# Performance work log

Hardware: AMD Instinct MI355X
Metric: run time of the kernel (lower is better)

Reference implementation:

```python
import jax, jax.numpy as jnp
import numpy as np

N_NODES = 50000
N_EDGES = 800000
D_IN = 128
D_H = 128
N_LAYERS = 3
N_CLASSES = 10
NUM_GRAPHS = 256
BN_EPS = 1e-5


def _bn(h, gamma, beta):
    # BatchNorm1d, training-mode statistics (biased variance) over node axis
    mu = jnp.mean(h, axis=0)
    var = jnp.mean((h - mu) ** 2, axis=0)
    return (h - mu) * jax.lax.rsqrt(var + BN_EPS) * gamma + beta


def setup_inputs() -> dict:
    key = jax.random.key(0)
    ks = jax.random.split(key, 16)
    x = jax.random.normal(ks[0], (N_NODES, D_IN), dtype=jnp.float32)
    edge_index = jax.random.randint(ks[1], (2, N_EDGES), 0, N_NODES, dtype=jnp.int64)
    batch = jnp.sort(jax.random.randint(ks[2], (N_NODES,), 0, NUM_GRAPHS, dtype=jnp.int64))
    s1 = 1.0 / np.sqrt(D_IN)
    s2 = 1.0 / np.sqrt(D_H)
    W1 = jax.random.uniform(ks[3], (N_LAYERS, D_IN, D_H), jnp.float32, -s1, s1)
    b1 = jax.random.uniform(ks[4], (N_LAYERS, D_H), jnp.float32, -s1, s1)
    g1 = jnp.ones((N_LAYERS, D_H), jnp.float32)
    bt1 = jnp.zeros((N_LAYERS, D_H), jnp.float32)
    W2 = jax.random.uniform(ks[5], (N_LAYERS, D_H, D_H), jnp.float32, -s2, s2)
    b2 = jax.random.uniform(ks[6], (N_LAYERS, D_H), jnp.float32, -s2, s2)
    g2 = jnp.ones((N_LAYERS, D_H), jnp.float32)
    bt2 = jnp.zeros((N_LAYERS, D_H), jnp.float32)
    sc = 1.0 / np.sqrt(D_H * N_LAYERS)
    Wc1 = jax.random.uniform(ks[7], (D_H * N_LAYERS, D_H), jnp.float32, -sc, sc)
    bc1 = jax.random.uniform(ks[8], (D_H,), jnp.float32, -sc, sc)
    Wc2 = jax.random.uniform(ks[9], (D_H, N_CLASSES), jnp.float32, -s2, s2)
    bc2 = jax.random.uniform(ks[10], (N_CLASSES,), jnp.float32, -s2, s2)
    return {"x": x, "edge_index": edge_index, "batch": batch,
            "W1": W1, "b1": b1, "g1": g1, "bt1": bt1,
            "W2": W2, "b2": b2, "g2": g2, "bt2": bt2,
            "Wc1": Wc1, "bc1": bc1, "Wc2": Wc2, "bc2": bc2}


def reference(x, edge_index, batch, W1, b1, g1, bt1, W2, b2, g2, bt2, Wc1, bc1, Wc2, bc2):
    src = edge_index[0]
    dst = edge_index[1]
    readouts = []
    h = x
    for i in range(N_LAYERS):
        # GINConv, eps=0: (1+eps)*h + sum_{j->i} h_j, then MLP
        agg = jax.ops.segment_sum(h[src], dst, num_segments=N_NODES)  # [N, d]
        z = h + agg
        z = z @ W1[i] + b1[i]
        z = jax.nn.relu(_bn(z, g1[i], bt1[i]))
        z = z @ W2[i] + b2[i]
        # outer BN + ReLU
        h = jax.nn.relu(_bn(z, g2[i], bt2[i]))
        readouts.append(jax.ops.segment_sum(h, batch, num_segments=NUM_GRAPHS))
    h_graph = jnp.concatenate(readouts, axis=1)  # [G, L*d]
    # classifier (dropout in eval mode -> identity)
    out = jax.nn.relu(h_graph @ Wc1 + bc1) @ Wc2 + bc2
    return out
```

## Files before the change

### kernel.cpp

```cpp
#include <hip/hip_runtime.h>

#define N_NODES 50000
#define N_EDGES 800000
#define D 128
#define NLAYERS 3
#define N_CLASSES 10
#define NUM_GRAPHS 256
#define BN_EPS 1e-5f

#define CHUNKS 64
#define CHSIZE 12500
#define RANGES 4
#define RSIZE 12500
#define SBANKS 8
#define NBLK 196

typedef __attribute__((ext_vector_type(4))) float f4;
typedef __attribute__((ext_vector_type(2))) float f2;
typedef __attribute__((ext_vector_type(4))) int i4;
typedef __attribute__((ext_vector_type(8))) short short8;
typedef __attribute__((ext_vector_type(4))) unsigned short us4;
typedef __attribute__((ext_vector_type(8))) unsigned short us8;

__device__ inline float b2f(unsigned short u) {
    unsigned int i = ((unsigned int)u) << 16;
    return __builtin_bit_cast(float, i);
}
__device__ inline unsigned short f2b(float f) {
    unsigned int u = __builtin_bit_cast(unsigned int, f);
    unsigned int r = (u + 0x7FFFu + ((u >> 16) & 1u)) >> 16;
    return (unsigned short)r;
}

__device__ inline void coef_to_lds(const float* __restrict__ stats,
                                   const float* __restrict__ g,
                                   const float* __restrict__ bt,
                                   float* ac_sm, int tid) {
    if (tid < D) {
        float s = 0.f, q = 0.f;
#pragma unroll
        for (int b = 0; b < SBANKS; b++) {
            s += stats[b * 2 * D + tid];
            q += stats[b * 2 * D + D + tid];
        }
        float mu = s * (1.0f / N_NODES);
        float var = q * (1.0f / N_NODES) - mu * mu;
        float inv = rsqrtf(var + BN_EPS);
        float a = g[tid] * inv;
        ac_sm[tid] = a;
        ac_sm[D + tid] = bt[tid] - mu * a;
    }
}


__global__ __launch_bounds__(256) void k_ph(const int* __restrict__ dst,
                                            unsigned short* __restrict__ pos,
                                            unsigned short* __restrict__ ph) {
    __shared__ int h[RSIZE];
    int c = blockIdx.x, r = blockIdx.y;
    int t = threadIdx.x;
    for (int i = t; i < RSIZE; i += 256) h[i] = 0;
    __syncthreads();
    int base = c * CHSIZE;
    int lo = r * RSIZE;
    const i4* dst4 = (const i4*)(dst + base);
    for (int j = t; j < CHSIZE / 4; j += 256) {
        i4 dv = dst4[j];
#pragma unroll
        for (int u = 0; u < 4; u++) {
            int d = dv[u] - lo;
            if ((unsigned)d < RSIZE) pos[base + j * 4 + u] = (unsigned short)atomicAdd(&h[d], 1);
        }
    }
    __syncthreads();
    unsigned short* outp = ph + (size_t)c * N_NODES + lo;
    for (int i = t; i < RSIZE; i += 256) outp[i] = (unsigned short)h[i];
}

__global__ __launch_bounds__(256) void k_m1(unsigned short* __restrict__ ph,
                                            const int* __restrict__ bat,
                                            int* __restrict__ deg,
                                            int* __restrict__ bsum,
                                            int* __restrict__ gp,
                                            int* __restrict__ bh) {
    __shared__ int sm[256];
    __shared__ int hist[64];
    int t = threadIdx.x;
    if (t < 64) hist[t] = 0;
    int b = blockIdx.x * 256 + t;
    int s = 0;
    if (b < N_NODES) {
#pragma unroll 4
        for (int c = 0; c < CHUNKS; c++) {
            int v = ph[(size_t)c * N_NODES + b];
            ph[(size_t)c * N_NODES + b] = (unsigned short)s;
            s += v;
        }
        deg[b] = s;
    }
    sm[t] = s;
    __syncthreads();
    if (b < N_NODES) atomicAdd(&hist[min(s, 63)], 1);
    for (int off = 128; off > 0; off >>= 1) {
        if (t < off) sm[t] += sm[t + off];
        __syncthreads();
    }
    if (t == 0) bsum[blockIdx.x] = sm[0];
    if (t < 64) bh[blockIdx.x * 64 + t] = hist[t];
    if (b < N_NODES) {
        int bb = bat[b];
        int prev = (b == 0) ? -1 : bat[b - 1];
        for (int g = prev + 1; g <= bb; g++) gp[g] = b;
        if (b == N_NODES - 1)
            for (int g = bb + 1; g <= NUM_GRAPHS; g++) gp[g] = N_NODES;
    }
}


__global__ __launch_bounds__(256) void k_xw(const float* __restrict__ x,
                                            const float* __restrict__ W1,
                                            const float* __restrict__ W2,
                                            us4* __restrict__ xb,
                                            short8* __restrict__ Wb) {
    int gid = blockIdx.x * 256 + threadIdx.x;
    const f4* xf = (const f4*)x;
#pragma unroll
    for (int rep = 0; rep < 2; rep++) {
        int i = gid + rep * 800000;
        f4 v = xf[i];
        us4 o;
        o[0] = f2b(v.x); o[1] = f2b(v.y); o[2] = f2b(v.z); o[3] = f2b(v.w);
        xb[i] = o;
    }
    if (gid < 6 * 32 * 64) {
        int m = gid >> 11;
        int f = (gid >> 6) & 31;
        int l = gid & 63;
        int ct = f >> 2, ks = f & 3;
        int n = ct * 16 + (l & 15);
        int k0 = ks * 32 + (l >> 4) * 8;
        const float* Wsrc = (m < 3) ? (W1 + (size_t)m * D * D) : (W2 + (size_t)(m - 3) * D * D);
        short8 o;
#pragma unroll
        for (int j = 0; j < 8; j++) o[j] = (short)f2b(Wsrc[(size_t)(k0 + j) * D + n]);
        Wb[gid] = o;
    }
}


__global__ void k_s2(int* __restrict__ bsum, int* __restrict__ rowp, int* __restrict__ bh) {
    __shared__ int sm[256];
    int t = threadIdx.x;
    int v = (t < NBLK) ? bsum[t] : 0;
    sm[t] = v;
    __syncthreads();
    for (int off = 1; off < 256; off <<= 1) {
        int u = (t >= off) ? sm[t - off] : 0;
        __syncthreads();
        sm[t] += u;
        __syncthreads();
    }
    if (t < NBLK) bsum[t] = sm[t] - v;
    if (t == NBLK - 1) rowp[N_NODES] = sm[t];
    __syncthreads();
    int tot = 0;
    if (t < 64) {
        for (int blk = 0; blk < NBLK; blk++) tot += bh[blk * 64 + t];
    }
    sm[t] = (t < 64) ? tot : 0;
    __syncthreads();
    for (int off = 1; off < 64; off <<= 1) {
        int u = (t >= off && t < 64) ? sm[t - off] : 0;
        __syncthreads();
        if (t < 64) sm[t] += u;
        __syncthreads();
    }
    if (t < 64) {
        int run = sm[t] - tot;
        for (int blk = 0; blk < NBLK; blk++) {
            int tmp = bh[blk * 64 + t];
            bh[blk * 64 + t] = run;
            run += tmp;
        }
    }
}


__global__ void k_s3(const int* __restrict__ deg, const int* __restrict__ bsum,
                     int* __restrict__ rowp, const int* __restrict__ bh,
                     unsigned short* __restrict__ perm) {
    __shared__ int sm[256];
    __shared__ int lh[64];
    int t = threadIdx.x;
    if (t < 64) lh[t] = 0;
    int i = blockIdx.x * 256 + t;
    int v = (i < N_NODES) ? deg[i] : 0;
    sm[t] = v;
    __syncthreads();
    for (int off = 1; off < 256; off <<= 1) {
        int u = (t >= off) ? sm[t - off] : 0;
        __syncthreads();
        sm[t] += u;
        __syncthreads();
    }
    if (i < N_NODES) {
        rowp[i] = bsum[blockIdx.x] + sm[t] - v;
        int bk = min(v, 63);
        int p = atomicAdd(&lh[bk], 1);
        perm[bh[blockIdx.x * 64 + bk] + p] = (unsigned short)i;
    }
}

__global__ __launch_bounds__(256) void k_scatter(const int* __restrict__ src,
                                                 const int* __restrict__ dst,
                                                 const unsigned short* __restrict__ pos,
                                                 const unsigned short* __restrict__ ph,
                                                 const int* __restrict__ rowp,
                                                 unsigned short* __restrict__ csr) {
    int e0 = (blockIdx.x * 256 + threadIdx.x) * 4;
    if (e0 >= N_EDGES) return;
    i4 sv = *(const i4*)(src + e0);
    i4 dv = *(const i4*)(dst + e0);
    us4 pv = *(const us4*)(pos + e0);
#pragma unroll
    for (int u = 0; u < 4; u++) {
        int cc = (e0 + u) / CHSIZE;
        int d = dv[u];
        csr[rowp[d] + (int)ph[(size_t)cc * N_NODES + d] + (int)pv[u]] = (unsigned short)sv[u];
    }
}


template <bool APPLY_T>
__global__ __launch_bounds__(256) void k_agg(const us8* __restrict__ H,
                                             const float* __restrict__ stats,
                                             const float* __restrict__ g,
                                             const float* __restrict__ bt,
                                             const int* __restrict__ rowp,
                                             const unsigned short* __restrict__ csr,
                                             const unsigned short* __restrict__ perm,
                                             us8* __restrict__ U) {
    __shared__ float ac_sm[2 * D];
    int tid = threadIdx.x;
    if (APPLY_T) {
        coef_to_lds(stats, g, bt, ac_sm, tid);
        __syncthreads();
    }
    int gid = blockIdx.x * 256 + tid;
    int node = perm[gid >> 4];
    int lane = tid & 15;
    float av[8], cv[8];
    if (APPLY_T) {
#pragma unroll
        for (int i = 0; i < 8; i++) {
            av[i] = ac_sm[lane * 8 + i];
            cv[i] = ac_sm[D + lane * 8 + i];
        }
    }
    float s[8] = {0.f, 0.f, 0.f, 0.f, 0.f, 0.f, 0.f, 0.f};
    auto accum = [&](us8 v) {
#pragma unroll
        for (int i = 0; i < 8; i++) {
            float f = b2f(v[i]);
            if (APPLY_T) f = fmaxf(f * av[i] + cv[i], 0.f);
            s[i] += f;
        }
    };
    accum(H[(size_t)node * 16 + lane]);
    int beg = rowp[node], end = rowp[node + 1];
    int j = beg;
    for (; j + 8 <= end; j += 8) {
        int idx[8];
#pragma unroll
        for (int u = 0; u < 8; u++) idx[u] = csr[j + u];
        us8 v[8];
#pragma unroll
        for (int u = 0; u < 8; u++) v[u] = H[(size_t)idx[u] * 16 + lane];
#pragma unroll
        for (int u = 0; u < 8; u++) accum(v[u]);
    }
    for (; j + 2 <= end; j += 2) {
        int i0 = csr[j], i1 = csr[j + 1];
        us8 v0 = H[(size_t)i0 * 16 + lane];
        us8 v1 = H[(size_t)i1 * 16 + lane];
        accum(v0); accum(v1);
    }
    if (j < end) accum(H[(size_t)csr[j] * 16 + lane]);
    us8 o;
#pragma unroll
    for (int i = 0; i < 8; i++) o[i] = f2b(s[i]);
    U[(size_t)node * 16 + lane] = o;
}


template <bool TRANS>
__global__ __launch_bounds__(256) void k_gemm(const unsigned short* __restrict__ A,
                                              const short8* __restrict__ Wb,
                                              const float* __restrict__ bias,
                                              const float* __restrict__ stats_in,
                                              const float* __restrict__ g,
                                              const float* __restrict__ bt,
                                              unsigned short* __restrict__ Z,
                                              float* __restrict__ stats_out, int M) {
    __shared__ float lds_s[D], lds_q[D];
    __shared__ float ac_sm[2 * D];
    int tid = threadIdx.x;
    if (tid < D) { lds_s[tid] = 0.f; lds_q[tid] = 0.f; }
    if (TRANS) coef_to_lds(stats_in, g, bt, ac_sm, tid);
    int w = tid >> 6, l = tid & 63;
    int lr = l & 15, lg = l >> 4;
    int rowb0 = blockIdx.x * 128 + w * 32;
    f4 acc[2][8];
#pragma unroll
    for (int ct = 0; ct < 8; ct++) {
        float bv = bias[ct * 16 + lr];
#pragma unroll
        for (int rt = 0; rt < 2; rt++) {
            acc[rt][ct].x = bv; acc[rt][ct].y = bv; acc[rt][ct].z = bv; acc[rt][ct].w = bv;
        }
    }
    __syncthreads();

#pragma unroll
    for (int ks = 0; ks < 4; ks++) {
        short8 a[2];
#pragma unroll
        for (int rt = 0; rt < 2; rt++) {
            int arow = rowb0 + rt * 16 + lr;
            int arow_c = arow < M ? arow : M - 1;
            if (!TRANS) {
                a[rt] = *(const short8*)(A + (size_t)arow_c * D + ks * 32 + lg * 8);
            } else {
                int k0 = ks * 32 + lg * 8;
                const unsigned short* ap = A + (size_t)arow_c * D + k0;
                us4 v0 = *(const us4*)ap;
                us4 v1 = *(const us4*)(ap + 4);
                f4 a0 = *(const f4*)&ac_sm[k0];
                f4 a1 = *(const f4*)&ac_sm[k0 + 4];
                f4 c0 = *(const f4*)&ac_sm[D + k0];
                f4 c1 = *(const f4*)&ac_sm[D + k0 + 4];
                a[rt][0] = (short)f2b(fmaxf(b2f(v0[0]) * a0.x + c0.x, 0.f));
                a[rt][1] = (short)f2b(fmaxf(b2f(v0[1]) * a0.y + c0.y, 0.f));
                a[rt][2] = (short)f2b(fmaxf(b2f(v0[2]) * a0.z + c0.z, 0.f));
                a[rt][3] = (short)f2b(fmaxf(b2f(v0[3]) * a0.w + c0.w, 0.f));
                a[rt][4] = (short)f2b(fmaxf(b2f(v1[0]) * a1.x + c1.x, 0.f));
                a[rt][5] = (short)f2b(fmaxf(b2f(v1[1]) * a1.y + c1.y, 0.f));
                a[rt][6] = (short)f2b(fmaxf(b2f(v1[2]) * a1.z + c1.z, 0.f));
                a[rt][7] = (short)f2b(fmaxf(b2f(v1[3]) * a1.w + c1.w, 0.f));
            }
        }
#pragma unroll
        for (int ct = 0; ct < 8; ct++) {
            short8 b = Wb[(ct * 4 + ks) * 64 + l];
            acc[0][ct] = __builtin_amdgcn_mfma_f32_16x16x32_bf16(a[0], b, acc[0][ct], 0, 0, 0);
            acc[1][ct] = __builtin_amdgcn_mfma_f32_16x16x32_bf16(a[1], b, acc[1][ct], 0, 0, 0);
        }
    }

#pragma unroll
    for (int ct = 0; ct < 8; ct++) {
        float s = 0.f, q = 0.f;
#pragma unroll
        for (int rt = 0; rt < 2; rt++) {
#pragma unroll
            for (int r = 0; r < 4; r++) {
                float v = acc[rt][ct][r];
                int rd = rowb0 + rt * 16 + lg * 4 + r;
                float m = rd < M ? 1.f : 0.f;
                s += v * m;
                q += v * v * m;
                if (rd < M) Z[(size_t)rd * D + ct * 16 + lr] = f2b(v);
            }
        }
        s += __shfl_xor(s, 16);
        s += __shfl_xor(s, 32);
        q += __shfl_xor(q, 16);
        q += __shfl_xor(q, 32);
        if (lg == 0) {
            atomicAdd(&lds_s[ct * 16 + lr], s);
            atomicAdd(&lds_q[ct * 16 + lr], q);
        }
    }
    __syncthreads();
    int bank = blockIdx.x & (SBANKS - 1);
    if (tid < D) {
        atomicAdd(&stats_out[bank * 2 * D + tid], lds_s[tid]);
        atomicAdd(&stats_out[bank * 2 * D + D + tid], lds_q[tid]);
    }
}


__global__ __launch_bounds__(256) void k_readout(const unsigned int* __restrict__ Zb,
                                                 const float* __restrict__ stats,
                                                 const float* __restrict__ g,
                                                 const float* __restrict__ bt,
                                                 const int* __restrict__ gp,
                                                 const int* __restrict__ batch,
                                                 float* __restrict__ ro, int layer) {
    __shared__ f2 sm[256];
    __shared__ float ac_sm[2 * D];
    int tid = threadIdx.x;
    coef_to_lds(stats, g, bt, ac_sm, tid);
    __syncthreads();
    int n0 = blockIdx.x * 256;
    int n1 = n0 + 256; if (n1 > N_NODES) n1 = N_NODES;
    int g_lo = batch[n0], g_hi = batch[n1 - 1];
    int grp = tid >> 6, cw = tid & 63;
    float a0 = ac_sm[2 * cw], a1 = ac_sm[2 * cw + 1];
    float c0 = ac_sm[D + 2 * cw], c1 = ac_sm[D + 2 * cw + 1];
    for (int gg = g_lo; gg <= g_hi; gg++) {
        int beg = gp[gg]; if (beg < n0) beg = n0;
        int end = gp[gg + 1]; if (end > n1) end = n1;
        f2 acc; acc.x = 0.f; acc.y = 0.f;
        for (int r = beg + grp; r < end; r += 4) {
            unsigned int v = Zb[(size_t)r * 64 + cw];
            float x0 = b2f((unsigned short)(v & 0xFFFFu));
            float x1 = b2f((unsigned short)(v >> 16));
            acc.x += fmaxf(x0 * a0 + c0, 0.f);
            acc.y += fmaxf(x1 * a1 + c1, 0.f);
        }
        sm[tid] = acc;
        __syncthreads();
        if (tid < 64) {
            f2 t = sm[tid];
            t.x += sm[tid + 64].x + sm[tid + 128].x + sm[tid + 192].x;
            t.y += sm[tid + 64].y + sm[tid + 128].y + sm[tid + 192].y;
            atomicAdd(&ro[(size_t)gg * (NLAYERS * D) + layer * D + 2 * cw], t.x);
            atomicAdd(&ro[(size_t)gg * (NLAYERS * D) + layer * D + 2 * cw + 1], t.y);
        }
        __syncthreads();
    }
}


__global__ void k_cls(const float* __restrict__ ro, const float* __restrict__ Wc1,
                      const float* __restrict__ bc1, const float* __restrict__ Wc2,
                      const float* __restrict__ bc2, float* __restrict__ out) {
    __shared__ float r_sm[NLAYERS * D];
    __shared__ float h_sm[D];
    int g = blockIdx.x;
    int t = threadIdx.x;
    for (int i = t; i < NLAYERS * D; i += D) r_sm[i] = ro[(size_t)g * (NLAYERS * D) + i];
    __syncthreads();
    float acc = bc1[t];
    for (int k = 0; k < NLAYERS * D; k++) acc += r_sm[k] * Wc1[(size_t)k * D + t];
    h_sm[t] = fmaxf(acc, 0.f);
    __syncthreads();
    if (t < N_CLASSES) {
        float o = bc2[t];
        for (int k = 0; k < D; k++) o += h_sm[k] * Wc2[k * N_CLASSES + t];
        out[g * N_CLASSES + t] = o;
    }
}


extern "C" void kernel_launch(void* const* d_in, const int* in_sizes, int n_in,
                              void* d_out, int out_size, void* d_ws, size_t ws_size,
                              hipStream_t stream) {
    const float* x   = (const float*)d_in[0];
    const int*   ei  = (const int*)d_in[1];
    const int*   bat = (const int*)d_in[2];
    const float* W1  = (const float*)d_in[3];
    const float* b1  = (const float*)d_in[4];
    const float* g1  = (const float*)d_in[5];
    const float* bt1 = (const float*)d_in[6];
    const float* W2  = (const float*)d_in[7];
    const float* b2  = (const float*)d_in[8];
    const float* g2  = (const float*)d_in[9];
    const float* bt2 = (const float*)d_in[10];
    const float* Wc1 = (const float*)d_in[11];
    const float* bc1 = (const float*)d_in[12];
    const float* Wc2 = (const float*)d_in[13];
    const float* bc2 = (const float*)d_in[14];
    float* out = (float*)d_out;

    const int* src = ei;
    const int* dst = ei + N_EDGES;

    char* ws = (char*)d_ws;
    size_t off = 0;
    auto alloc = [&](size_t bytes) -> void* {
        void* p = ws + off;
        off += (bytes + 255) & ~(size_t)255;
        return p;
    };
    float* stats = (float*)alloc(6 * SBANKS * 2 * D * sizeof(float));
    float* ro    = (float*)alloc((size_t)NUM_GRAPHS * NLAYERS * D * sizeof(float));
    size_t zero_bytes = off;
    int*   deg   = (int*)alloc(N_NODES * sizeof(int));
    int*   gp    = (int*)alloc((NUM_GRAPHS + 1) * sizeof(int));
    int*   bsum  = (int*)alloc(256 * sizeof(int));
    int*   rowp  = (int*)alloc((N_NODES + 1) * sizeof(int));
    int*   bh    = (int*)alloc(NBLK * 64 * sizeof(int));
    unsigned short* pos  = (unsigned short*)alloc(N_EDGES * sizeof(unsigned short));
    unsigned short* csr  = (unsigned short*)alloc(N_EDGES * sizeof(unsigned short));
    unsigned short* perm = (unsigned short*)alloc(N_NODES * sizeof(unsigned short));
    const size_t NBH = (size_t)N_NODES * D * sizeof(unsigned short);
    unsigned short* xb   = (unsigned short*)alloc(NBH);
    unsigned short* bufA = (unsigned short*)alloc(NBH);
    unsigned short* bufB = (unsigned short*)alloc(NBH);
    unsigned short* bufC = (unsigned short*)alloc(NBH);
    short8* Wb   = (short8*)alloc(6 * 32 * 64 * sizeof(short8));
    unsigned short* ph = (unsigned short*)bufB;

    hipMemsetAsync(ws, 0, zero_bytes, stream);

    k_ph<<<dim3(CHUNKS, RANGES), 256, 0, stream>>>(dst, pos, ph);
    k_m1<<<NBLK, 256, 0, stream>>>(ph, bat, deg, bsum, gp, bh);
    k_xw<<<3125, 256, 0, stream>>>(x, W1, W2, (us4*)xb, Wb);
    k_s2<<<1, 256, 0, stream>>>(bsum, rowp, bh);
    k_s3<<<NBLK, 256, 0, stream>>>(deg, bsum, rowp, bh, perm);
    k_scatter<<<(N_EDGES / 4 + 255) / 256, 256, 0, stream>>>(src, dst, pos, ph, rowp, csr);

    const int agg_grid  = N_NODES * 16 / 256;
    const int gemm_grid = (N_NODES + 127) / 128;
    const unsigned short* H = xb;
    for (int i = 0; i < NLAYERS; i++) {
        float* st1 = stats + (size_t)(2 * i) * SBANKS * 2 * D;
        float* st2 = stats + (size_t)(2 * i + 1) * SBANKS * 2 * D;
        float* st2p = stats + (size_t)(2 * i - 1) * SBANKS * 2 * D;
        if (i == 0)
            k_agg<false><<<agg_grid, 256, 0, stream>>>((const us8*)H, nullptr, nullptr, nullptr,
                                                       rowp, csr, perm, (us8*)bufA);
        else
            k_agg<true><<<agg_grid, 256, 0, stream>>>((const us8*)H, st2p, g2 + (i - 1) * D,
                                                      bt2 + (i - 1) * D, rowp, csr, perm, (us8*)bufA);
        k_gemm<false><<<gemm_grid, 256, 0, stream>>>(bufA, Wb + (size_t)i * 2048, b1 + i * D,
                                                     nullptr, nullptr, nullptr, bufB, st1, N_NODES);
        k_gemm<true><<<gemm_grid, 256, 0, stream>>>(bufB, Wb + (size_t)(3 + i) * 2048, b2 + i * D,
                                                    st1, g1 + i * D, bt1 + i * D, bufC, st2, N_NODES);
        k_readout<<<NBLK, 256, 0, stream>>>((const unsigned int*)bufC, st2, g2 + i * D, bt2 + i * D,
                                            gp, bat, ro, i);
        H = bufC;
    }
    k_cls<<<NUM_GRAPHS, 128, 0, stream>>>(ro, Wc1, bc1, Wc2, bc2, out);
}
```

Measured before the change: 334.2 us.

## Fuse neighbor aggregation with first MLP GEMM via LDS tile

Merges the aggregation kernel and the first GEMM of each layer into one kernel. Each block aggregates 128 nodes in perm order into an LDS tile, then runs MFMA on that tile, scatters rows to their original node positions, and accumulates batch-norm statistics. This removes one launch per layer and the round trip of the aggregated buffer through global memory. In exchange, the output writes become scattered, 128 nodes are aggregated per block with less parallelism, and LDS use grows. The scatter kernel also hoists the chunk index computation out of its loop.

```diff
diff --git a/kernel.cpp b/kernel.cpp
--- a/kernel.cpp
+++ b/kernel.cpp
@@ -14,6 +14,7 @@
 #define RSIZE 12500
 #define SBANKS 8
 #define NBLK 196
+#define UP 136
 
 typedef __attribute__((ext_vector_type(4))) float f4;
 typedef __attribute__((ext_vector_type(2))) float f2;
@@ -219,36 +220,41 @@
                                                  unsigned short* __restrict__ csr) {
     int e0 = (blockIdx.x * 256 + threadIdx.x) * 4;
     if (e0 >= N_EDGES) return;
+    int cc = e0 / CHSIZE;
     i4 sv = *(const i4*)(src + e0);
     i4 dv = *(const i4*)(dst + e0);
     us4 pv = *(const us4*)(pos + e0);
+    const unsigned short* phc = ph + (size_t)cc * N_NODES;
 #pragma unroll
     for (int u = 0; u < 4; u++) {
-        int cc = (e0 + u) / CHSIZE;
         int d = dv[u];
-        csr[rowp[d] + (int)ph[(size_t)cc * N_NODES + d] + (int)pv[u]] = (unsigned short)sv[u];
+        csr[rowp[d] + (int)phc[d] + (int)pv[u]] = (unsigned short)sv[u];
     }
 }
 
 
 template <bool APPLY_T>
-__global__ __launch_bounds__(256) void k_agg(const us8* __restrict__ H,
-                                             const float* __restrict__ stats,
-                                             const float* __restrict__ g,
-                                             const float* __restrict__ bt,
-                                             const int* __restrict__ rowp,
-                                             const unsigned short* __restrict__ csr,
-                                             const unsigned short* __restrict__ perm,
-                                             us8* __restrict__ U) {
+__global__ __launch_bounds__(256) void k_ag(const us8* __restrict__ H,
+                                            const float* __restrict__ stats,
+                                            const float* __restrict__ g,
+                                            const float* __restrict__ bt,
+                                            const int* __restrict__ rowp,
+                                            const unsigned short* __restrict__ csr,
+                                            const unsigned short* __restrict__ perm,
+                                            const short8* __restrict__ Wb,
+                                            const float* __restrict__ bias,
+                                            unsigned short* __restrict__ Z,
+                                            float* __restrict__ stats_out) {
+    __shared__ unsigned short u[128][UP];
     __shared__ float ac_sm[2 * D];
+    __shared__ float lds_s[D], lds_q[D];
     int tid = threadIdx.x;
-    if (APPLY_T) {
-        coef_to_lds(stats, g, bt, ac_sm, tid);
-        __syncthreads();
-    }
-    int gid = blockIdx.x * 256 + tid;
-    int node = perm[gid >> 4];
-    int lane = tid & 15;
+    if (tid < D) { lds_s[tid] = 0.f; lds_q[tid] = 0.f; }
+    if (APPLY_T) coef_to_lds(stats, g, bt, ac_sm, tid);
+    __syncthreads();
+
+    int slot = tid >> 4, lane = tid & 15;
+    int base = blockIdx.x * 128;
     float av[8], cv[8];
     if (APPLY_T) {
 #pragma unroll
@@ -257,56 +263,128 @@
             cv[i] = ac_sm[D + lane * 8 + i];
         }
     }
-    float s[8] = {0.f, 0.f, 0.f, 0.f, 0.f, 0.f, 0.f, 0.f};
-    auto accum = [&](us8 v) {
-#pragma unroll
-        for (int i = 0; i < 8; i++) {
-            float f = b2f(v[i]);
-            if (APPLY_T) f = fmaxf(f * av[i] + cv[i], 0.f);
-            s[i] += f;
-        }
-    };
-    accum(H[(size_t)node * 16 + lane]);
-    int beg = rowp[node], end = rowp[node + 1];
-    int j = beg;
-    for (; j + 8 <= end; j += 8) {
-        int idx[8];
-#pragma unroll
-        for (int u = 0; u < 8; u++) idx[u] = csr[j + u];
-        us8 v[8];
-#pragma unroll
-        for (int u = 0; u < 8; u++) v[u] = H[(size_t)idx[u] * 16 + lane];
-#pragma unroll
-        for (int u = 0; u < 8; u++) accum(v[u]);
-    }
-    for (; j + 2 <= end; j += 2) {
-        int i0 = csr[j], i1 = csr[j + 1];
-        us8 v0 = H[(size_t)i0 * 16 + lane];
-        us8 v1 = H[(size_t)i1 * 16 + lane];
-        accum(v0); accum(v1);
-    }
-    if (j < end) accum(H[(size_t)csr[j] * 16 + lane]);
-    us8 o;
-#pragma unroll
-    for (int i = 0; i < 8; i++) o[i] = f2b(s[i]);
-    U[(size_t)node * 16 + lane] = o;
-}
-
-
-template <bool TRANS>
-__global__ __launch_bounds__(256) void k_gemm(const unsigned short* __restrict__ A,
-                                              const short8* __restrict__ Wb,
-                                              const float* __restrict__ bias,
-                                              const float* __restrict__ stats_in,
-                                              const float* __restrict__ g,
-                                              const float* __restrict__ bt,
-                                              unsigned short* __restrict__ Z,
-                                              float* __restrict__ stats_out, int M) {
+    for (int ns = 0; ns < 8; ns++) {
+        int li = base + ns * 16 + slot;
+        int node = perm[li < N_NODES ? li : N_NODES - 1];
+        float s[8] = {0.f, 0.f, 0.f, 0.f, 0.f, 0.f, 0.f, 0.f};
+        auto accum = [&](us8 v) {
+#pragma unroll
+            for (int i = 0; i < 8; i++) {
+                float f = b2f(v[i]);
+                if (APPLY_T) f = fmaxf(f * av[i] + cv[i], 0.f);
+                s[i] += f;
+            }
+        };
+        accum(H[(size_t)node * 16 + lane]);
+        int beg = rowp[node], end = rowp[node + 1];
+        int j = beg;
+        for (; j + 8 <= end; j += 8) {
+            int idx[8];
+#pragma unroll
+            for (int q = 0; q < 8; q++) idx[q] = csr[j + q];
+            us8 v[8];
+#pragma unroll
+            for (int q = 0; q < 8; q++) v[q] = H[(size_t)idx[q] * 16 + lane];
+#pragma unroll
+            for (int q = 0; q < 8; q++) accum(v[q]);
+        }
+        for (; j + 2 <= end; j += 2) {
+            int i0 = csr[j], i1 = csr[j + 1];
+            us8 v0 = H[(size_t)i0 * 16 + lane];
+            us8 v1 = H[(size_t)i1 * 16 + lane];
+            accum(v0); accum(v1);
+        }
+        if (j < end) accum(H[(size_t)csr[j] * 16 + lane]);
+        us8 o;
+#pragma unroll
+        for (int i = 0; i < 8; i++) o[i] = f2b(s[i]);
+        *(us8*)&u[ns * 16 + slot][lane * 8] = o;
+    }
+    __syncthreads();
+
+    int w = tid >> 6, l = tid & 63;
+    int lr = l & 15, lg = l >> 4;
+    int rowb0 = w * 32;
+    f4 acc[2][8];
+#pragma unroll
+    for (int ct = 0; ct < 8; ct++) {
+        float bv = bias[ct * 16 + lr];
+#pragma unroll
+        for (int rt = 0; rt < 2; rt++) {
+            acc[rt][ct].x = bv; acc[rt][ct].y = bv; acc[rt][ct].z = bv; acc[rt][ct].w = bv;
+        }
+    }
+#pragma unroll
+    for (int ks = 0; ks < 4; ks++) {
+        int k0 = ks * 32 + lg * 8;
+        short8 a[2];
+#pragma unroll
+        for (int rt = 0; rt < 2; rt++)
+            a[rt] = *(const short8*)&u[rowb0 + rt * 16 + lr][k0];
+#pragma unroll
+        for (int ct = 0; ct < 8; ct++) {
+            short8 b = Wb[(ct * 4 + ks) * 64 + l];
+            acc[0][ct] = __builtin_amdgcn_mfma_f32_16x16x32_bf16(a[0], b, acc[0][ct], 0, 0, 0);
+            acc[1][ct] = __builtin_amdgcn_mfma_f32_16x16x32_bf16(a[1], b, acc[1][ct], 0, 0, 0);
+        }
+    }
+
+    float vm[2][4];
+    int nrow[2][4];
+#pragma unroll
+    for (int rt = 0; rt < 2; rt++)
+#pragma unroll
+        for (int r = 0; r < 4; r++) {
+            int gi = base + rowb0 + rt * 16 + lg * 4 + r;
+            bool ok = gi < N_NODES;
+            vm[rt][r] = ok ? 1.f : 0.f;
+            nrow[rt][r] = ok ? (int)perm[gi] : 0;
+        }
+#pragma unroll
+    for (int ct = 0; ct < 8; ct++) {
+        float s = 0.f, q = 0.f;
+#pragma unroll
+        for (int rt = 0; rt < 2; rt++) {
+#pragma unroll
+            for (int r = 0; r < 4; r++) {
+                float v = acc[rt][ct][r];
+                s += v * vm[rt][r];
+                q += v * v * vm[rt][r];
+                if (vm[rt][r] != 0.f)
+                    Z[(size_t)nrow[rt][r] * D + ct * 16 + lr] = f2b(v);
+            }
+        }
+        s += __shfl_xor(s, 16);
+        s += __shfl_xor(s, 32);
+        q += __shfl_xor(q, 16);
+        q += __shfl_xor(q, 32);
+        if (lg == 0) {
+            atomicAdd(&lds_s[ct * 16 + lr], s);
+            atomicAdd(&lds_q[ct * 16 + lr], q);
+        }
+    }
+    __syncthreads();
+    int bank = blockIdx.x & (SBANKS - 1);
+    if (tid < D) {
+        atomicAdd(&stats_out[bank * 2 * D + tid], lds_s[tid]);
+        atomicAdd(&stats_out[bank * 2 * D + D + tid], lds_q[tid]);
+    }
+}
+
+
+__global__ __launch_bounds__(256) void k_gemm2(const unsigned short* __restrict__ A,
+                                               const short8* __restrict__ Wb,
+                                               const float* __restrict__ bias,
+                                               const float* __restrict__ stats_in,
+                                               const float* __restrict__ g,
+                                               const float* __restrict__ bt,
+                                               unsigned short* __restrict__ Z,
+                                               float* __restrict__ stats_out, int M) {
     __shared__ float lds_s[D], lds_q[D];
     __shared__ float ac_sm[2 * D];
     int tid = threadIdx.x;
     if (tid < D) { lds_s[tid] = 0.f; lds_q[tid] = 0.f; }
-    if (TRANS) coef_to_lds(stats_in, g, bt, ac_sm, tid);
+    coef_to_lds(stats_in, g, bt, ac_sm, tid);
     int w = tid >> 6, l = tid & 63;
     int lr = l & 15, lg = l >> 4;
     int rowb0 = blockIdx.x * 128 + w * 32;
@@ -328,26 +406,22 @@
         for (int rt = 0; rt < 2; rt++) {
             int arow = rowb0 + rt * 16 + lr;
             int arow_c = arow < M ? arow : M - 1;
-            if (!TRANS) {
-                a[rt] = *(const short8*)(A + (size_t)arow_c * D + ks * 32 + lg * 8);
-            } else {
-                int k0 = ks * 32 + lg * 8;
-                const unsigned short* ap = A + (size_t)arow_c * D + k0;
-                us4 v0 = *(const us4*)ap;
-                us4 v1 = *(const us4*)(ap + 4);
-                f4 a0 = *(const f4*)&ac_sm[k0];
-                f4 a1 = *(const f4*)&ac_sm[k0 + 4];
-                f4 c0 = *(const f4*)&ac_sm[D + k0];
-                f4 c1 = *(const f4*)&ac_sm[D + k0 + 4];
-                a[rt][0] = (short)f2b(fmaxf(b2f(v0[0]) * a0.x + c0.x, 0.f));
-                a[rt][1] = (short)f2b(fmaxf(b2f(v0[1]) * a0.y + c0.y, 0.f));
-                a[rt][2] = (short)f2b(fmaxf(b2f(v0[2]) * a0.z + c0.z, 0.f));
-                a[rt][3] = (short)f2b(fmaxf(b2f(v0[3]) * a0.w + c0.w, 0.f));
-                a[rt][4] = (short)f2b(fmaxf(b2f(v1[0]) * a1.x + c1.x, 0.f));
-                a[rt][5] = (short)f2b(fmaxf(b2f(v1[1]) * a1.y + c1.y, 0.f));
-                a[rt][6] = (short)f2b(fmaxf(b2f(v1[2]) * a1.z + c1.z, 0.f));
-                a[rt][7] = (short)f2b(fmaxf(b2f(v1[3]) * a1.w + c1.w, 0.f));
-            }
+            int k0 = ks * 32 + lg * 8;
+            const unsigned short* ap = A + (size_t)arow_c * D + k0;
+            us4 v0 = *(const us4*)ap;
+            us4 v1 = *(const us4*)(ap + 4);
+            f4 a0 = *(const f4*)&ac_sm[k0];
+            f4 a1 = *(const f4*)&ac_sm[k0 + 4];
+            f4 c0 = *(const f4*)&ac_sm[D + k0];
+            f4 c1 = *(const f4*)&ac_sm[D + k0 + 4];
+            a[rt][0] = (short)f2b(fmaxf(b2f(v0[0]) * a0.x + c0.x, 0.f));
+            a[rt][1] = (short)f2b(fmaxf(b2f(v0[1]) * a0.y + c0.y, 0.f));
+            a[rt][2] = (short)f2b(fmaxf(b2f(v0[2]) * a0.z + c0.z, 0.f));
+            a[rt][3] = (short)f2b(fmaxf(b2f(v0[3]) * a0.w + c0.w, 0.f));
+            a[rt][4] = (short)f2b(fmaxf(b2f(v1[0]) * a1.x + c1.x, 0.f));
+            a[rt][5] = (short)f2b(fmaxf(b2f(v1[1]) * a1.y + c1.y, 0.f));
+            a[rt][6] = (short)f2b(fmaxf(b2f(v1[2]) * a1.z + c1.z, 0.f));
+            a[rt][7] = (short)f2b(fmaxf(b2f(v1[3]) * a1.w + c1.w, 0.f));
         }
 #pragma unroll
         for (int ct = 0; ct < 8; ct++) {
@@ -497,7 +571,6 @@
     unsigned short* perm = (unsigned short*)alloc(N_NODES * sizeof(unsigned short));
     const size_t NBH = (size_t)N_NODES * D * sizeof(unsigned short);
     unsigned short* xb   = (unsigned short*)alloc(NBH);
-    unsigned short* bufA = (unsigned short*)alloc(NBH);
     unsigned short* bufB = (unsigned short*)alloc(NBH);
     unsigned short* bufC = (unsigned short*)alloc(NBH);
     short8* Wb   = (short8*)alloc(6 * 32 * 64 * sizeof(short8));
@@ -512,7 +585,7 @@
     k_s3<<<NBLK, 256, 0, stream>>>(deg, bsum, rowp, bh, perm);
     k_scatter<<<(N_EDGES / 4 + 255) / 256, 256, 0, stream>>>(src, dst, pos, ph, rowp, csr);
 
-    const int agg_grid  = N_NODES * 16 / 256;
+    const int ag_grid   = (N_NODES + 127) / 128;
     const int gemm_grid = (N_NODES + 127) / 128;
     const unsigned short* H = xb;
     for (int i = 0; i < NLAYERS; i++) {
@@ -520,15 +593,15 @@
         float* st2 = stats + (size_t)(2 * i + 1) * SBANKS * 2 * D;
         float* st2p = stats + (size_t)(2 * i - 1) * SBANKS * 2 * D;
         if (i == 0)
-            k_agg<false><<<agg_grid, 256, 0, stream>>>((const us8*)H, nullptr, nullptr, nullptr,
-                                                       rowp, csr, perm, (us8*)bufA);
+            k_ag<false><<<ag_grid, 256, 0, stream>>>((const us8*)H, nullptr, nullptr, nullptr,
+                                                     rowp, csr, perm, Wb + (size_t)i * 2048,
+                                                     b1 + i * D, bufB, st1);
         else
-            k_agg<true><<<agg_grid, 256, 0, stream>>>((const us8*)H, st2p, g2 + (i - 1) * D,
-                                                      bt2 + (i - 1) * D, rowp, csr, perm, (us8*)bufA);
-        k_gemm<false><<<gemm_grid, 256, 0, stream>>>(bufA, Wb + (size_t)i * 2048, b1 + i * D,
-                                                     nullptr, nullptr, nullptr, bufB, st1, N_NODES);
-        k_gemm<true><<<gemm_grid, 256, 0, stream>>>(bufB, Wb + (size_t)(3 + i) * 2048, b2 + i * D,
-                                                    st1, g1 + i * D, bt1 + i * D, bufC, st2, N_NODES);
+            k_ag<true><<<ag_grid, 256, 0, stream>>>((const us8*)H, st2p, g2 + (i - 1) * D,
+                                                    bt2 + (i - 1) * D, rowp, csr, perm,
+                                                    Wb + (size_t)i * 2048, b1 + i * D, bufB, st1);
+        k_gemm2<<<gemm_grid, 256, 0, stream>>>(bufB, Wb + (size_t)(3 + i) * 2048, b2 + i * D,
+                                               st1, g1 + i * D, bt1 + i * D, bufC, st2, N_NODES);
         k_readout<<<NBLK, 256, 0, stream>>>((const unsigned int*)bufC, st2, g2 + i * D, bt2 + i * D,
                                             gp, bat, ro, i);
         H = bufC;
```

Result: slower. 376.4 us (+12.6%).
